# Kernel optimization log

Hardware: AMD Instinct MI355X
Metric: run time of the kernel (lower is better)

## Reference

```python
import jax, jax.numpy as jnp
import numpy as np

B = 128          # batch
T = 196          # total_patches per view (2 views -> 2*T tokens)
ENC = 1024       # encoder_embed_dim
DEC = 512        # decoder_embed_dim
V = 98           # num unmasked (visible) tokens per sample
M = 2 * T - V    # num masked tokens (294)


def setup_inputs() -> dict:
    key = jax.random.key(0)
    kx, kperm, kw, kmt, kpos, kview = jax.random.split(key, 6)
    x = jax.random.normal(kx, (B, V, ENC), jnp.float32)
    # masked_ids: unique ids per row in [0, 2T) — built from permutations
    perms = jax.vmap(jax.random.permutation, in_axes=(0, None))(
        jax.random.split(kperm, B), 2 * T)
    masked_ids = perms[:, :M].astype(jnp.int64)
    W = jax.random.normal(kw, (DEC, ENC), jnp.float32) * 0.02
    b = jnp.zeros((DEC,), jnp.float32)
    mask_token = jax.random.normal(kmt, (1, 1, DEC), jnp.float32)
    pos_embed = jax.random.normal(kpos, (1, 2 * T, DEC), jnp.float32)
    view_embed = jax.random.normal(kview, (2, DEC), jnp.float32)
    return {"x": x, "masked_ids": masked_ids, "W": W, "b": b,
            "mask_token": mask_token, "pos_embed": pos_embed,
            "view_embed": view_embed}


def reference(x, masked_ids, W, b, mask_token, pos_embed, view_embed):
    Bn = x.shape[0]
    # Linear: enc -> dec
    xp = jnp.einsum('bve,de->bvd', x, W) + b          # (B, V, DEC)
    # visible ids = sorted complement of masked_ids (vectorized, no batch loop)
    rows = jnp.arange(Bn)[:, None]
    vis_mask = jnp.ones((Bn, 2 * T), bool).at[rows, masked_ids].set(False)
    # stable argsort puts True(visible, ~mask=False) positions first, in order
    visible_ids = jnp.argsort(~vis_mask, axis=1)[:, :V]  # (B, V)
    # scatter projected visible tokens into mask-token placeholders
    base = jnp.broadcast_to(mask_token, (Bn, 2 * T, DEC))
    view = base.at[rows, visible_ids].set(xp)          # (B, 2T, DEC)
    # per-view embedding: first T tokens -> view 0, last T -> view 1
    ve = jnp.concatenate([
        jnp.broadcast_to(view_embed[0], (T, DEC)),
        jnp.broadcast_to(view_embed[1], (T, DEC))], axis=0)  # (2T, DEC)
    return view + pos_embed + ve[None, :, :]
```

## Files before the change

kernel.cpp:

```cpp
#include <hip/hip_runtime.h>

#define BATCH 128
#define VIS   98
#define TOK   196
#define TOK2  392
#define ENC   1024
#define DEC   512
#define MSK   294

#define NXB 6272
#define NWB 256

typedef __bf16 bf16x8 __attribute__((ext_vector_type(8)));
typedef float  f32x4  __attribute__((ext_vector_type(4)));

__device__ __forceinline__ unsigned short f2bf(float f) {
    union { float f; unsigned u; } c; c.f = f;
    unsigned u = c.u;
    return (unsigned short)((u + 0x7fffu + ((u >> 16) & 1u)) >> 16);
}

__device__ __forceinline__ void g2lds16(const void* gptr, void* lptr) {
    __builtin_amdgcn_global_load_lds(
        (const __attribute__((address_space(1))) void*)gptr,
        (__attribute__((address_space(3))) void*)lptr, 16, 0, 0);
}

__global__ __launch_bounds__(512) void setup(const float* __restrict__ x,
                                             const float* __restrict__ W,
                                             const int* __restrict__ mids,
                                             unsigned short* __restrict__ xb,
                                             unsigned short* __restrict__ wbm,
                                             int* __restrict__ visids,
                                             unsigned char* __restrict__ flags) {
    int bid = blockIdx.x, tid = threadIdx.x;
    if (bid < NXB + NWB) {
        const float* src = (bid < NXB) ? x : W;
        unsigned short* dst = (bid < NXB) ? xb : wbm;
        int i = (bid < NXB ? bid : bid - NXB) * 512 + tid;
        float4 f = ((const float4*)src)[i];
        ushort4 o;
        o.x = f2bf(f.x); o.y = f2bf(f.y); o.z = f2bf(f.z); o.w = f2bf(f.w);
        ((ushort4*)dst)[i] = o;
        return;
    }
    int b = bid - NXB - NWB;
    __shared__ unsigned char lf[TOK2];
    __shared__ int wtot[8];
    if (tid < TOK2) lf[tid] = 1;
    __syncthreads();
    if (tid < MSK) lf[mids[b * MSK + tid]] = 0;
    __syncthreads();
    int flag = (tid < TOK2) ? (int)lf[tid] : 0;
    unsigned long long bal = __ballot(flag != 0);
    int lane = tid & 63, wv = tid >> 6;
    int pre = __popcll(bal & ((1ull << lane) - 1ull));
    if (lane == 0) wtot[wv] = __popcll(bal);
    __syncthreads();
    int off = 0;
    for (int i = 0; i < wv; ++i) off += wtot[i];
    if (flag) visids[b * VIS + off + pre] = tid;
    if (tid < TOK2) flags[b * TOK2 + tid] = lf[tid];
}

__global__ __launch_bounds__(256) void fill_masked(const unsigned char* __restrict__ flags,
                                                   const float* __restrict__ mask_token,
                                                   const float* __restrict__ pos,
                                                   const float* __restrict__ ve,
                                                   float* __restrict__ out) {
    int b = blockIdx.y;
    int g = blockIdx.x * 256 + threadIdx.x;
    int t  = g >> 7;
    int d4 = g & 127;
    int tok = b * TOK2 + t;
    if (flags[tok]) return;
    float4 m = ((const float4*)mask_token)[d4];
    float4 p = ((const float4*)(pos + (size_t)t * DEC))[d4];
    float4 v = ((const float4*)(ve + (t >= TOK ? DEC : 0)))[d4];
    float4 r;
    r.x = m.x + p.x + v.x;
    r.y = m.y + p.y + v.y;
    r.z = m.z + p.z + v.z;
    r.w = m.w + p.w + v.w;
    ((float4*)(out + (size_t)tok * DEC))[d4] = r;
}

__global__ __launch_bounds__(256, 4) void gemm_scatter(
    const unsigned short* __restrict__ xb,
    const unsigned short* __restrict__ wb,
    const float* __restrict__ bias,
    const float* __restrict__ pos,
    const float* __restrict__ ve,
    const int* __restrict__ vis,
    float* __restrict__ out) {
    __shared__ unsigned short As[64 * 64];
    __shared__ unsigned short Bs[128 * 64];
    __shared__ int rowdst[64];
    __shared__ int rowt[64];

    int tid = threadIdx.x;
    int lane = tid & 63, w = tid >> 6;
    int l16 = lane & 15, q = lane >> 4;
    int wm = w & 1, wn = w >> 1;
    int m0 = blockIdx.y * 64, n0 = blockIdx.x * 128;

    if (tid < 64) {
        int gr = m0 + tid;
        int t = vis[gr];
        rowt[tid] = t;
        rowdst[tid] = (gr / VIS) * TOK2 + t;
    }

    int c = (tid & 7) ^ ((tid >> 3) & 7);
    const unsigned short* gA = xb + (size_t)(m0 + (tid >> 3)) * ENC + c * 8;
    const unsigned short* gB = wb + (size_t)(n0 + (tid >> 3)) * ENC + c * 8;
    char* ldsA = (char*)As + tid * 16;
    char* ldsB = (char*)Bs + tid * 16;

    f32x4 acc[2][4];
    #pragma unroll
    for (int i = 0; i < 2; ++i)
        #pragma unroll
        for (int j = 0; j < 4; ++j)
            acc[i][j] = (f32x4){0.f, 0.f, 0.f, 0.f};

    for (int k0 = 0; k0 < ENC; k0 += 64) {
        __syncthreads();
        #pragma unroll
        for (int t = 0; t < 2; ++t)
            g2lds16(gA + (size_t)t * 32 * ENC + k0, ldsA + t * 4096);
        #pragma unroll
        for (int t = 0; t < 4; ++t)
            g2lds16(gB + (size_t)t * 32 * ENC + k0, ldsB + t * 4096);
        __syncthreads();

        #pragma unroll
        for (int u = 0; u < 2; ++u) {
            int slot = ((u * 4 + q) ^ (l16 & 7)) * 16;
            bf16x8 bfrag[4], afrag[2];
            #pragma unroll
            for (int j = 0; j < 4; ++j)
                bfrag[j] = *(const bf16x8*)((const char*)Bs + (wn * 64 + j * 16 + l16) * 128 + slot);
            #pragma unroll
            for (int i = 0; i < 2; ++i)
                afrag[i] = *(const bf16x8*)((const char*)As + (wm * 32 + i * 16 + l16) * 128 + slot);
            #pragma unroll
            for (int i = 0; i < 2; ++i)
                #pragma unroll
                for (int j = 0; j < 4; ++j)
                    acc[i][j] = __builtin_amdgcn_mfma_f32_16x16x32_bf16(afrag[i], bfrag[j], acc[i][j], 0, 0, 0);
        }
    }

    #pragma unroll
    for (int j = 0; j < 4; ++j) {
        int gcol = n0 + wn * 64 + j * 16 + l16;
        float bc = bias[gcol];
        float v0 = ve[gcol];
        float v1 = ve[DEC + gcol];
        #pragma unroll
        for (int i = 0; i < 2; ++i) {
            #pragma unroll
            for (int r = 0; r < 4; ++r) {
                int rl = wm * 32 + i * 16 + q * 4 + r;
                int t = rowt[rl];
                float val = acc[i][j][r] + bc + pos[(size_t)t * DEC + gcol]
                          + (t >= TOK ? v1 : v0);
                out[(size_t)rowdst[rl] * DEC + gcol] = val;
            }
        }
    }
}

extern "C" void kernel_launch(void* const* d_in, const int* in_sizes, int n_in,
                              void* d_out, int out_size, void* d_ws, size_t ws_size,
                              hipStream_t stream) {
    (void)in_sizes; (void)n_in; (void)out_size; (void)ws_size;
    const float* x    = (const float*)d_in[0];
    const int*   mids = (const int*)d_in[1];
    const float* W    = (const float*)d_in[2];
    const float* bias = (const float*)d_in[3];
    const float* mt   = (const float*)d_in[4];
    const float* pos  = (const float*)d_in[5];
    const float* ve   = (const float*)d_in[6];
    float* out = (float*)d_out;

    unsigned short* xb = (unsigned short*)d_ws;
    unsigned short* wbm = xb + (size_t)BATCH * VIS * ENC;
    int* visids = (int*)(wbm + (size_t)DEC * ENC);
    unsigned char* flags = (unsigned char*)(visids + BATCH * VIS);

    hipLaunchKernelGGL(setup, dim3(NXB + NWB + BATCH), dim3(512), 0, stream,
                       x, W, mids, xb, wbm, visids, flags);
    hipLaunchKernelGGL(fill_masked, dim3(TOK2 * 128 / 256, BATCH), dim3(256), 0, stream,
                       flags, mt, pos, ve, out);
    hipLaunchKernelGGL(gemm_scatter, dim3(4, (BATCH * VIS) / 64), dim3(256), 0, stream,
                       xb, wbm, bias, pos, ve, visids, out);
}
```

Measured before the change: 185.2 us.

## Fuse masked-token fill into setup kernel and swizzle GEMM block order

Removes the separate fill_masked launch by adding blocks to the setup kernel that write masked tokens directly from masked_ids, without the flags buffer or a full-grid pass that skipped visible tokens. Each fill block handles 32 masked tokens with coalesced float4 writes. The GEMM grid is flattened to 1D with a grouped block remap so that nearby blocks share A and B tiles in cache. This saves one launch and the flags round trip, at the cost of a larger, more heterogeneous setup grid.

```diff
diff --git a/kernel.cpp b/kernel.cpp
--- a/kernel.cpp
+++ b/kernel.cpp
@@ -10,6 +10,9 @@
 
 #define NXB 6272
 #define NWB 256
+#define NFILL 1176
+
+#define NGEMM 784
 
 typedef __bf16 bf16x8 __attribute__((ext_vector_type(8)));
 typedef float  f32x4  __attribute__((ext_vector_type(4)));
@@ -26,13 +29,17 @@
         (__attribute__((address_space(3))) void*)lptr, 16, 0, 0);
 }
 
-__global__ __launch_bounds__(512) void setup(const float* __restrict__ x,
-                                             const float* __restrict__ W,
-                                             const int* __restrict__ mids,
-                                             unsigned short* __restrict__ xb,
-                                             unsigned short* __restrict__ wbm,
-                                             int* __restrict__ visids,
-                                             unsigned char* __restrict__ flags) {
+__global__ __launch_bounds__(512) void setup_fill(
+    const float* __restrict__ x,
+    const float* __restrict__ W,
+    const int* __restrict__ mids,
+    const float* __restrict__ mask_token,
+    const float* __restrict__ pos,
+    const float* __restrict__ ve,
+    unsigned short* __restrict__ xb,
+    unsigned short* __restrict__ wbm,
+    int* __restrict__ visids,
+    float* __restrict__ out) {
     int bid = blockIdx.x, tid = threadIdx.x;
     if (bid < NXB + NWB) {
         const float* src = (bid < NXB) ? x : W;
@@ -44,45 +51,52 @@
         ((ushort4*)dst)[i] = o;
         return;
     }
-    int b = bid - NXB - NWB;
-    __shared__ unsigned char lf[TOK2];
-    __shared__ int wtot[8];
-    if (tid < TOK2) lf[tid] = 1;
+    if (bid < NXB + NWB + BATCH) {
+        int b = bid - NXB - NWB;
+        __shared__ unsigned char lf[TOK2];
+        __shared__ int wtot[8];
+        if (tid < TOK2) lf[tid] = 1;
+        __syncthreads();
+        if (tid < MSK) lf[mids[b * MSK + tid]] = 0;
+        __syncthreads();
+        int flag = (tid < TOK2) ? (int)lf[tid] : 0;
+        unsigned long long bal = __ballot(flag != 0);
+        int lane = tid & 63, wv = tid >> 6;
+        int pre = __popcll(bal & ((1ull << lane) - 1ull));
+        if (lane == 0) wtot[wv] = __popcll(bal);
+        __syncthreads();
+        int off = 0;
+        for (int i = 0; i < wv; ++i) off += wtot[i];
+        if (flag) visids[b * VIS + off + pre] = tid;
+        return;
+    }
+    int fb = bid - (NXB + NWB + BATCH);
+    __shared__ int base[32];
+    __shared__ int tsl[32];
+    if (tid < 32) {
+        int fid = fb * 32 + tid;
+        int b = fid / MSK;
+        int t = mids[fid];
+        tsl[tid] = t;
+        base[tid] = (b * TOK2 + t) * 128;
+    }
     __syncthreads();
-    if (tid < MSK) lf[mids[b * MSK + tid]] = 0;
-    __syncthreads();
-    int flag = (tid < TOK2) ? (int)lf[tid] : 0;
-    unsigned long long bal = __ballot(flag != 0);
-    int lane = tid & 63, wv = tid >> 6;
-    int pre = __popcll(bal & ((1ull << lane) - 1ull));
-    if (lane == 0) wtot[wv] = __popcll(bal);
-    __syncthreads();
-    int off = 0;
-    for (int i = 0; i < wv; ++i) off += wtot[i];
-    if (flag) visids[b * VIS + off + pre] = tid;
-    if (tid < TOK2) flags[b * TOK2 + tid] = lf[tid];
-}
-
-__global__ __launch_bounds__(256) void fill_masked(const unsigned char* __restrict__ flags,
-                                                   const float* __restrict__ mask_token,
-                                                   const float* __restrict__ pos,
-                                                   const float* __restrict__ ve,
-                                                   float* __restrict__ out) {
-    int b = blockIdx.y;
-    int g = blockIdx.x * 256 + threadIdx.x;
-    int t  = g >> 7;
-    int d4 = g & 127;
-    int tok = b * TOK2 + t;
-    if (flags[tok]) return;
-    float4 m = ((const float4*)mask_token)[d4];
-    float4 p = ((const float4*)(pos + (size_t)t * DEC))[d4];
-    float4 v = ((const float4*)(ve + (t >= TOK ? DEC : 0)))[d4];
-    float4 r;
-    r.x = m.x + p.x + v.x;
-    r.y = m.y + p.y + v.y;
-    r.z = m.z + p.z + v.z;
-    r.w = m.w + p.w + v.w;
-    ((float4*)(out + (size_t)tok * DEC))[d4] = r;
+    float4 m = ((const float4*)mask_token)[tid & 127];
+    #pragma unroll
+    for (int i = 0; i < 8; ++i) {
+        int g = i * 512 + tid;
+        int ltok = g >> 7;
+        int d4 = tid & 127;
+        int t = tsl[ltok];
+        float4 p = ((const float4*)pos)[t * 128 + d4];
+        float4 v = ((const float4*)(ve + (t >= TOK ? DEC : 0)))[d4];
+        float4 r;
+        r.x = m.x + p.x + v.x;
+        r.y = m.y + p.y + v.y;
+        r.z = m.z + p.z + v.z;
+        r.w = m.w + p.w + v.w;
+        ((float4*)out)[base[ltok] + d4] = r;
+    }
 }
 
 __global__ __launch_bounds__(256, 4) void gemm_scatter(
@@ -98,11 +112,16 @@
     __shared__ int rowdst[64];
     __shared__ int rowt[64];
 
+    int bid = blockIdx.x;
     int tid = threadIdx.x;
     int lane = tid & 63, w = tid >> 6;
     int l16 = lane & 15, q = lane >> 4;
     int wm = w & 1, wn = w >> 1;
-    int m0 = blockIdx.y * 64, n0 = blockIdx.x * 128;
+
+    int mb, nb;
+    if (bid < 768) { mb = (bid & 7) + ((bid >> 5) << 3); nb = (bid >> 3) & 3; }
+    else           { int ii = bid - 768; mb = 192 + (ii & 3); nb = ii >> 2; }
+    int m0 = mb * 64, n0 = nb * 128;
 
     if (tid < 64) {
         int gr = m0 + tid;
@@ -188,12 +207,9 @@
     unsigned short* xb = (unsigned short*)d_ws;
     unsigned short* wbm = xb + (size_t)BATCH * VIS * ENC;
     int* visids = (int*)(wbm + (size_t)DEC * ENC);
-    unsigned char* flags = (unsigned char*)(visids + BATCH * VIS);
-
-    hipLaunchKernelGGL(setup, dim3(NXB + NWB + BATCH), dim3(512), 0, stream,
-                       x, W, mids, xb, wbm, visids, flags);
-    hipLaunchKernelGGL(fill_masked, dim3(TOK2 * 128 / 256, BATCH), dim3(256), 0, stream,
-                       flags, mt, pos, ve, out);
-    hipLaunchKernelGGL(gemm_scatter, dim3(4, (BATCH * VIS) / 64), dim3(256), 0, stream,
+
+    hipLaunchKernelGGL(setup_fill, dim3(NXB + NWB + BATCH + NFILL), dim3(512), 0, stream,
+                       x, W, mids, mt, pos, ve, xb, wbm, visids, out);
+    hipLaunchKernelGGL(gemm_scatter, dim3(NGEMM), dim3(256), 0, stream,
                        xb, wbm, bias, pos, ve, visids, out);
 }
```

Result: faster. 178.9 us (-3.4%).
